# Performance work log

Measured on AMD Instinct MI355X. Metric: run time of the kernel, lower is better.

## Reference

```python
import jax, jax.numpy as jnp
import numpy as np

SEQ, INP, BOND, BATCH = 256, 4, 128, 2048


def setup_inputs() -> dict:
    key = jax.random.key(0)
    k1, k2, k3 = jax.random.split(key, 3)
    # near-eye init: identity plus small noise (matches near_eye_init intent)
    eye = jnp.eye(BOND, dtype=jnp.float32)
    core_tensors = eye[None, None] + 0.01 * jax.random.normal(k1, (SEQ, INP, BOND, BOND), dtype=jnp.float32)
    edge_vecs = jax.random.normal(k2, (2, BOND), dtype=jnp.float32) / np.float32(np.sqrt(BOND))
    input_data = jax.random.randint(k3, (SEQ, BATCH), 0, INP)
    return {"input_data": input_data, "core_tensors": core_tensors, "edge_vecs": edge_vecs}


def reference(input_data, core_tensors, edge_vecs):
    """log P(x) = 2*log|h_n^T omega| - log Z for an open-boundary real MPS.

    h_t = A_t[x_t] h_{t-1}, h_0 = alpha.
    Z tracked via density-matrix recurrence M_t = sum_i A_t[i] M_{t-1} A_t[i]^T,
    M_0 = alpha alpha^T, Z = omega^T M_n omega.
    Log-scaling on both scans prevents under/overflow.
    """
    alpha, omega = edge_vecs[0], edge_vecs[1]
    B = input_data.shape[1]
    D = core_tensors.shape[2]

    # ---- amplitude scan over sequence (batched D-dim matvecs) ----
    def amp_step(carry, inp):
        h, logn = carry            # h: [B, D], logn: [B]
        A_t, x_t = inp             # A_t: [I, D, D], x_t: [B]
        mats = A_t[x_t]            # [B, D, D] gather of per-token core slices
        h = jnp.einsum('bij,bj->bi', mats, h)
        s = jnp.linalg.norm(h, axis=-1, keepdims=True)
        return (h / s, logn + jnp.log(s[:, 0])), None

    h0 = jnp.broadcast_to(alpha, (B, D))
    (h, logn), _ = jax.lax.scan(amp_step, (h0, jnp.zeros((B,), h0.dtype)),
                                (core_tensors, input_data))
    amp = h @ omega                                   # [B]
    log_amp_sq = 2.0 * (jnp.log(jnp.abs(amp)) + logn)

    # ---- normalization scan (transfer-matrix / density-matrix form) ----
    def z_step(carry, A_t):
        M, logz = carry            # M: [D, D]
        M = jnp.einsum('iab,bc,idc->ad', A_t, M, A_t)  # sum_i A_i M A_i^T
        s = jnp.linalg.norm(M)
        return (M / s, logz + jnp.log(s)), None

    M0 = jnp.outer(alpha, alpha)
    (M, logz), _ = jax.lax.scan(z_step, (M0, jnp.zeros((), M0.dtype)), core_tensors)
    log_Z = jnp.log(omega @ M @ omega) + logz

    return log_amp_sq - log_Z
```

## Files before the change

### kernel.cpp

```cpp
#include <hip/hip_runtime.h>
#include <cstdint>
#include <cstddef>

#define SEQ   256
#define INP   4
#define BOND  128
#define BATCH 2048
#define MATSZ (BOND*BOND)

typedef __bf16 bf16x8 __attribute__((ext_vector_type(8)));
typedef __bf16 bf16x4 __attribute__((ext_vector_type(4)));
typedef float  f32x4  __attribute__((ext_vector_type(4)));
typedef short  s16x4  __attribute__((ext_vector_type(4)));

static constexpr size_t SZ_MAT   = (size_t)SEQ*INP*MATSZ*2;
static constexpr size_t OFF_ABF  = 0;
static constexpr size_t OFF_ATBF = OFF_ABF + SZ_MAT;
static constexpr size_t OFF_BHI  = OFF_ATBF + SZ_MAT;
static constexpr size_t OFF_BLO  = OFF_BHI + SZ_MAT;
static constexpr size_t SZ_MWS   = 2ull*MATSZ*2;
static constexpr size_t SZ_TAIL  = SZ_MWS + (size_t)BATCH*4 + 64;

static __device__ __forceinline__ unsigned short f2bf(float f) {
    union { float f; uint32_t u; } v; v.f = f;
    uint32_t r = (v.u + 0x7FFFu + ((v.u >> 16) & 1u)) >> 16;
    return (unsigned short)r;
}
static __device__ __forceinline__ float bf2f(unsigned short b) {
    union { uint32_t u; float f; } v; v.u = ((uint32_t)b) << 16;
    return v.f;
}
static __device__ __forceinline__ f32x4 mfma16(bf16x8 a, bf16x8 b, f32x4 c) {
    return __builtin_amdgcn_mfma_f32_16x16x32_bf16(a, b, c, 0, 0, 0);
}
#if defined(__has_builtin)
#if __has_builtin(__builtin_amdgcn_mfma_f32_16x16x16bf16_1k)
#define HAVE_MFMA16X16_BUILTIN 1
#endif
#endif
static __device__ __forceinline__ f32x4 mfma16x16(bf16x4 a, bf16x4 b, f32x4 c) {
#ifdef HAVE_MFMA16X16_BUILTIN
    return __builtin_amdgcn_mfma_f32_16x16x16bf16_1k(
        __builtin_bit_cast(s16x4, a), __builtin_bit_cast(s16x4, b), c, 0, 0, 0);
#else
    asm("v_mfma_f32_16x16x16_bf16 %0, %1, %2, %0" : "+v"(c) : "v"(a), "v"(b));
    return c;
#endif
}
static __device__ __forceinline__ unsigned int cvtpk(float a, float b) {
    unsigned int d;
    asm("v_cvt_pk_bf16_f32 %0, %1, %2" : "=v"(d) : "v"(a), "v"(b));
    return d;
}
static __device__ __forceinline__ int xoff(int r, int c8) {
    return ((r << 4) + (c8 ^ (r & 15))) << 3;
}
static __device__ __forceinline__ void gload_lds16(const unsigned short* g, unsigned short* l) {
    __builtin_amdgcn_global_load_lds((const __attribute__((address_space(1))) unsigned int*)g,
                                     (__attribute__((address_space(3))) unsigned int*)l,
                                     16, 0, 0);
}
static __device__ __forceinline__ void stage_mat(const unsigned short* __restrict__ Ai,
                                                 unsigned short* dst, int tid) {
#pragma unroll
    for (int j = 0; j < 4; ++j) {
        int slot = j * 512 + tid;
        int r = slot >> 4, c8 = slot & 15;
        const unsigned short* src = Ai + (size_t)r * BOND + ((c8 ^ (r & 15)) << 3);
        unsigned short* ldst = dst + (size_t)(j * 512 + (tid & ~63)) * 8;
        gload_lds16(src, ldst);
    }
}

__global__ void convert_kernel(const float* __restrict__ core,
                               unsigned short* __restrict__ abf,
                               unsigned short* __restrict__ atbf,
                               unsigned short* __restrict__ bhi,
                               unsigned short* __restrict__ blo,
                               int use_blo) {
    __shared__ unsigned short tile[BOND][BOND + 2];
    const int mat = blockIdx.x;
    const float* src = core + (size_t)mat * MATSZ;
    unsigned short* dA = abf  + (size_t)mat * MATSZ;
    unsigned short* dT = atbf + (size_t)mat * MATSZ;
    unsigned short* dH = bhi  + (size_t)mat * MATSZ;
    unsigned short* dL = blo  + (size_t)mat * MATSZ;
    const int tid = threadIdx.x;
    for (int j = 0; j < 16; ++j) {
        int lin4 = (tid + j * 256) * 4;
        float4 f = *(const float4*)(src + lin4);
        int r = lin4 >> 7, c = lin4 & 127;
        unsigned short a0=f2bf(f.x), a1=f2bf(f.y), a2=f2bf(f.z), a3=f2bf(f.w);
        *(ushort4*)(dA + lin4) = make_ushort4(a0,a1,a2,a3);
        tile[r][c]=a0; tile[r][c+1]=a1; tile[r][c+2]=a2; tile[r][c+3]=a3;
        float b0 = f.x - ((r == c    ) ? 1.0f : 0.0f);
        float b1 = f.y - ((r == c + 1) ? 1.0f : 0.0f);
        float b2 = f.z - ((r == c + 2) ? 1.0f : 0.0f);
        float b3 = f.w - ((r == c + 3) ? 1.0f : 0.0f);
        unsigned short h0=f2bf(b0), h1=f2bf(b1), h2=f2bf(b2), h3=f2bf(b3);
        *(ushort4*)(dH + lin4) = make_ushort4(h0,h1,h2,h3);
        if (use_blo) {
            *(ushort4*)(dL + lin4) = make_ushort4(
                f2bf(b0 - bf2f(h0)), f2bf(b1 - bf2f(h1)),
                f2bf(b2 - bf2f(h2)), f2bf(b3 - bf2f(h3)));
        }
    }
    __syncthreads();
    for (int j = 0; j < 16; ++j) {
        int lin4 = (tid + j * 256) * 4;
        int co = lin4 >> 7, r0 = lin4 & 127;
        *(ushort4*)(dT + lin4) = make_ushort4(tile[r0][co], tile[r0+1][co],
                                              tile[r0+2][co], tile[r0+3][co]);
    }
}

struct ZSm {
    unsigned short As[2][MATSZ];
    unsigned short M[MATSZ];
    float vec[BOND];
};
struct ASm2 {
    int   toks[SEQ * 32];
    unsigned short hhi[32 * BOND];
    unsigned short hlo[32 * BOND];
    float partial[8][32];
    float sinv[32];
    float logn[32];
};
union SmU { ZSm z; ASm2 a; };

template<int USE_BLO>
__global__ __launch_bounds__(512)
__attribute__((amdgpu_waves_per_eu(2, 2)))
void main_kernel(
        const int*   __restrict__ xdata,
        const float* __restrict__ edge,
        const unsigned short* __restrict__ abf,
        const unsigned short* __restrict__ atbf,
        const unsigned short* __restrict__ bhi,
        const unsigned short* __restrict__ blo,
        unsigned short* __restrict__ mws,
        float* __restrict__ logamp) {
    __shared__ SmU sm;
    const int tid = threadIdx.x;
    const int l   = tid & 63;
    const int w   = tid >> 6;
    const int lo  = l & 15;
    const int hi  = l >> 4;

    if (blockIdx.x < 2) {
        const int chain = blockIdx.x;
        const unsigned short* Abase = chain ? atbf : abf;

        if (tid < BOND) sm.z.vec[tid] = edge[chain * BOND + tid];
        __syncthreads();
        for (int idx = tid; idx < MATSZ; idx += 512) {
            int r = idx >> 7, c = idx & 127;
            sm.z.M[xoff(r, c >> 3) + (c & 7)] = f2bf(sm.z.vec[r] * sm.z.vec[c]);
        }
        stage_mat(Abase + (size_t)(chain ? (SEQ - 1) : 0) * INP * MATSZ, sm.z.As[0], tid);
        __syncthreads();

        int cur = 0;
        for (int s = 1; s <= 128; ++s) {
            const int tstep = chain ? (SEQ - s) : (s - 1);
            const unsigned short* As_g = Abase + (size_t)tstep * INP * MATSZ;
            f32x4 accM[2][8];
#pragma unroll
            for (int mt = 0; mt < 2; ++mt)
#pragma unroll
                for (int ct = 0; ct < 8; ++ct) accM[mt][ct] = (f32x4){0.f, 0.f, 0.f, 0.f};

            for (int i = 0; i < 4; ++i) {
                const unsigned short* nxt = nullptr;
                if (i < 3)           nxt = As_g + (size_t)(i + 1) * MATSZ;
                else if (s < 128)    nxt = Abase + (size_t)(chain ? (SEQ - s - 1) : s) * INP * MATSZ;
                if (nxt) stage_mat(nxt, sm.z.As[cur ^ 1], tid);

                if (w < 4) {
                    __builtin_amdgcn_s_setprio(1);
                    const unsigned short* Ac = sm.z.As[cur];
                    f32x4 acc1[8][2];
#pragma unroll
                    for (int pt = 0; pt < 8; ++pt) {
                        acc1[pt][0] = (f32x4){0.f, 0.f, 0.f, 0.f};
                        acc1[pt][1] = (f32x4){0.f, 0.f, 0.f, 0.f};
                    }
#pragma unroll
                    for (int kk = 0; kk < 4; ++kk) {
                        bf16x8 bq0 = *(const bf16x8*)&Ac[xoff(w * 32 + lo,      kk * 4 + hi)];
                        bf16x8 bq1 = *(const bf16x8*)&Ac[xoff(w * 32 + 16 + lo, kk * 4 + hi)];
#pragma unroll
                        for (int pt = 0; pt < 8; ++pt) {
                            bf16x8 mf = *(const bf16x8*)&sm.z.M[xoff(pt * 16 + lo, kk * 4 + hi)];
                            acc1[pt][0] = mfma16(mf, bq0, acc1[pt][0]);
                            acc1[pt][1] = mfma16(mf, bq1, acc1[pt][1]);
                        }
                    }
                    bf16x4 tf[2][8];
#pragma unroll
                    for (int pt = 0; pt < 8; ++pt)
#pragma unroll
                        for (int mt = 0; mt < 2; ++mt) {
                            union { unsigned int u[2]; bf16x4 v; } pk;
                            pk.u[0] = cvtpk(acc1[pt][mt][0], acc1[pt][mt][1]);
                            pk.u[1] = cvtpk(acc1[pt][mt][2], acc1[pt][mt][3]);
                            tf[mt][pt] = pk.v;
                        }
#pragma unroll
                    for (int ks = 0; ks < 8; ++ks) {
#pragma unroll
                        for (int ct = 0; ct < 8; ++ct) {
                            bf16x4 bb = *(const bf16x4*)&Ac[xoff(ct * 16 + lo, 2 * ks + (hi >> 1)) + 4 * (hi & 1)];
                            accM[0][ct] = mfma16x16(tf[0][ks], bb, accM[0][ct]);
                            accM[1][ct] = mfma16x16(tf[1][ks], bb, accM[1][ct]);
                        }
                    }
                    __builtin_amdgcn_s_setprio(0);
                }
                asm volatile("s_waitcnt vmcnt(0)" ::: "memory");
                __builtin_amdgcn_s_barrier();
                cur ^= 1;
            }
            if (w < 4) {
#pragma unroll
                for (int mt = 0; mt < 2; ++mt)
#pragma unroll
                    for (int ct = 0; ct < 8; ++ct)
#pragma unroll
                        for (int r = 0; r < 4; ++r) {
                            int row = w * 32 + mt * 16 + hi * 4 + r;
                            int col = ct * 16 + lo;
                            sm.z.M[xoff(row, col >> 3) + (col & 7)] =
                                f2bf(accM[mt][ct][r] * 0.25f);
                        }
            }
            asm volatile("s_waitcnt lgkmcnt(0)" ::: "memory");
            __builtin_amdgcn_s_barrier();
        }
        unsigned short* outb = mws + (size_t)chain * MATSZ;
        for (int j = 0; j < 4; ++j) {
            int chunk = tid + j * 512;
            int r = chunk >> 4, c8 = chunk & 15;
            *(bf16x8*)(outb + (size_t)r * BOND + c8 * 8) =
                *(const bf16x8*)&sm.z.M[xoff(r, c8)];
        }
    } else {
        const int lr = lo, lq = hi;
        const int b0 = (blockIdx.x - 2) * 32;

        for (int j = 0; j < 16; ++j) {
            int idx = tid + j * 512;
            int t = idx >> 5, c = idx & 31;
            sm.a.toks[idx] = xdata[(size_t)t * BATCH + b0 + c];
        }
        if (tid < 32) sm.a.logn[tid] = 0.f;
        for (int idx = tid; idx < 32 * BOND; idx += 512) {
            int c = idx >> 7, r = idx & 127;
            float v = edge[r];
            unsigned short hb = f2bf(v);
            int si = xoff(c, r >> 3) + (r & 7);
            sm.a.hhi[si] = hb;
            sm.a.hlo[si] = f2bf(v - bf2f(hb));
        }
        f32x4 al = *(const f32x4*)(edge + w * 16 + lq * 4);
        f32x4 hreg0 = al, hreg1 = al;
        __syncthreads();

        const size_t ro = (size_t)(w * 16 + lr) * BOND + lq * 8;

        bf16x8 bvh[4][4], bvl[4][4];
#pragma unroll
        for (int v = 0; v < 4; ++v)
#pragma unroll
            for (int kk = 0; kk < 4; ++kk) {
                bvh[v][kk] = *(const bf16x8*)(bhi + (size_t)v * MATSZ + ro + kk * 32);
                if (USE_BLO) bvl[v][kk] = *(const bf16x8*)(blo + (size_t)v * MATSZ + ro + kk * 32);
            }

        for (int t = 0; t < SEQ; ++t) {
            bf16x8 hh0[4], hh1[4], hl0[4], hl1[4];
#pragma unroll
            for (int kk = 0; kk < 4; ++kk) {
                hh0[kk] = *(const bf16x8*)&sm.a.hhi[xoff(lr,      kk * 4 + lq)];
                hh1[kk] = *(const bf16x8*)&sm.a.hhi[xoff(16 + lr, kk * 4 + lq)];
                hl0[kk] = *(const bf16x8*)&sm.a.hlo[xoff(lr,      kk * 4 + lq)];
                hl1[kk] = *(const bf16x8*)&sm.a.hlo[xoff(16 + lr, kk * 4 + lq)];
            }
            f32x4 acc[4][2];
#pragma unroll
            for (int v = 0; v < 4; ++v) {
                acc[v][0] = (f32x4){0.f, 0.f, 0.f, 0.f};
                acc[v][1] = (f32x4){0.f, 0.f, 0.f, 0.f};
            }
            const unsigned short* BhN = bhi + (size_t)(t + 1) * INP * MATSZ + ro;
            const unsigned short* BlN = blo + (size_t)(t + 1) * INP * MATSZ + ro;
#pragma unroll
            for (int v = 0; v < 4; ++v) {
#pragma unroll
                for (int kk = 0; kk < 4; ++kk) {
                    acc[v][0] = mfma16(bvh[v][kk], hh0[kk], acc[v][0]);
                    acc[v][0] = mfma16(bvh[v][kk], hl0[kk], acc[v][0]);
                    acc[v][1] = mfma16(bvh[v][kk], hh1[kk], acc[v][1]);
                    acc[v][1] = mfma16(bvh[v][kk], hl1[kk], acc[v][1]);
                    if (USE_BLO) {
                        acc[v][0] = mfma16(bvl[v][kk], hh0[kk], acc[v][0]);
                        acc[v][1] = mfma16(bvl[v][kk], hh1[kk], acc[v][1]);
                    }
                }
                if (t < SEQ - 1) {
#pragma unroll
                    for (int kk = 0; kk < 4; ++kk) {
                        bvh[v][kk] = *(const bf16x8*)(BhN + (size_t)v * MATSZ + kk * 32);
                        if (USE_BLO) bvl[v][kk] = *(const bf16x8*)(BlN + (size_t)v * MATSZ + kk * 32);
                    }
                }
            }
            int tokA = sm.a.toks[t * 32 + lr];
            int tokB = sm.a.toks[t * 32 + 16 + lr];
            f32x4 d0 = acc[0][0];
            d0 = (tokA == 1) ? acc[1][0] : d0;
            d0 = (tokA == 2) ? acc[2][0] : d0;
            d0 = (tokA == 3) ? acc[3][0] : d0;
            f32x4 d1 = acc[0][1];
            d1 = (tokB == 1) ? acc[1][1] : d1;
            d1 = (tokB == 2) ? acc[2][1] : d1;
            d1 = (tokB == 3) ? acc[3][1] : d1;
            f32x4 h2_0 = hreg0 + d0;
            f32x4 h2_1 = hreg1 + d1;

            if ((t & 7) == 7) {
                float ss0 = h2_0[0]*h2_0[0] + h2_0[1]*h2_0[1] + h2_0[2]*h2_0[2] + h2_0[3]*h2_0[3];
                ss0 += __shfl_xor(ss0, 16);
                ss0 += __shfl_xor(ss0, 32);
                float ss1 = h2_1[0]*h2_1[0] + h2_1[1]*h2_1[1] + h2_1[2]*h2_1[2] + h2_1[3]*h2_1[3];
                ss1 += __shfl_xor(ss1, 16);
                ss1 += __shfl_xor(ss1, 32);
                if (lq == 0) {
                    sm.a.partial[w][lr]      = ss0;
                    sm.a.partial[w][16 + lr] = ss1;
                }
                __syncthreads();
                if (tid < 32) {
                    float s2 = 0.f;
#pragma unroll
                    for (int w2 = 0; w2 < 8; ++w2) s2 += sm.a.partial[w2][tid];
                    sm.a.sinv[tid] = rsqrtf(s2);
                    sm.a.logn[tid] += 0.5f * logf(s2);
                }
                __syncthreads();
                h2_0 *= sm.a.sinv[lr];
                h2_1 *= sm.a.sinv[16 + lr];
            }
            hreg0 = h2_0;
            hreg1 = h2_1;
            __syncthreads();
#pragma unroll
            for (int ct = 0; ct < 2; ++ct) {
                f32x4 hv = (ct == 0) ? h2_0 : h2_1;
                int c = ct * 16 + lr;
                unsigned short q0 = f2bf(hv[0]), q1 = f2bf(hv[1]),
                               q2 = f2bf(hv[2]), q3 = f2bf(hv[3]);
                int c8w = w * 2 + (lq >> 1);
                int si  = xoff(c, c8w) + (lq & 1) * 4;
                *(ushort4*)&sm.a.hhi[si] = make_ushort4(q0, q1, q2, q3);
                *(ushort4*)&sm.a.hlo[si] =
                    make_ushort4(f2bf(hv[0] - bf2f(q0)), f2bf(hv[1] - bf2f(q1)),
                                 f2bf(hv[2] - bf2f(q2)), f2bf(hv[3] - bf2f(q3)));
            }
            __syncthreads();
        }
        f32x4 og = *(const f32x4*)(edge + BOND + w * 16 + lq * 4);
#pragma unroll
        for (int ct = 0; ct < 2; ++ct) {
            f32x4 hv = (ct == 0) ? hreg0 : hreg1;
            float ss = hv[0]*og[0] + hv[1]*og[1] + hv[2]*og[2] + hv[3]*og[3];
            ss += __shfl_xor(ss, 16);
            ss += __shfl_xor(ss, 32);
            if (lq == 0) sm.a.partial[w][ct * 16 + lr] = ss;
        }
        __syncthreads();
        if (tid < 32) {
            float dot = 0.f;
#pragma unroll
            for (int w2 = 0; w2 < 8; ++w2) dot += sm.a.partial[w2][tid];
            logamp[b0 + tid] = 2.f * (logf(fabsf(dot)) + sm.a.logn[tid]);
        }
    }
}

__global__ __launch_bounds__(1024) void fin_kernel(const unsigned short* __restrict__ mws,
                                                   const float* __restrict__ logamp,
                                                   float* __restrict__ out) {
    __shared__ float red[1024];
    const int tid = threadIdx.x;
    const unsigned short* Sf = mws;
    const unsigned short* Rb = mws + MATSZ;
    float part = 0.f;
    for (int j = 0; j < 16; ++j) {
        int idx = tid + j * 1024;
        part += bf2f(Sf[idx]) * bf2f(Rb[idx]);
    }
    red[tid] = part;
    __syncthreads();
    for (int off = 512; off > 0; off >>= 1) {
        if (tid < off) red[tid] += red[tid + off];
        __syncthreads();
    }
    float lz = logf(red[0]) + 256.0f * 1.3862943611198906f;
    out[tid]        = logamp[tid]        - lz;
    out[tid + 1024] = logamp[tid + 1024] - lz;
}

extern "C" void kernel_launch(void* const* d_in, const int* in_sizes, int n_in,
                              void* d_out, int out_size, void* d_ws, size_t ws_size,
                              hipStream_t stream) {
    const int*   xdata = (const int*)d_in[0];
    const float* core  = (const float*)d_in[1];
    const float* edge  = (const float*)d_in[2];
    float* out = (float*)d_out;
    char* ws = (char*)d_ws;

    const size_t need_full  = OFF_BLO + SZ_MAT + SZ_TAIL;
    const size_t need_noblo = OFF_BLO + SZ_TAIL;
    const int use_blo = (ws_size >= need_full) ? 1 : 0;
    if (!use_blo && ws_size < need_noblo) return;

    unsigned short* abf  = (unsigned short*)(ws + OFF_ABF);
    unsigned short* atbf = (unsigned short*)(ws + OFF_ATBF);
    unsigned short* bhi  = (unsigned short*)(ws + OFF_BHI);
    unsigned short* blo  = (unsigned short*)(ws + (use_blo ? OFF_BLO : OFF_BHI));
    const size_t tail = use_blo ? (OFF_BLO + SZ_MAT) : OFF_BLO;
    unsigned short* mws  = (unsigned short*)(ws + tail);
    float* logamp = (float*)(ws + tail + SZ_MWS);

    convert_kernel<<<SEQ * INP, 256, 0, stream>>>(core, abf, atbf, bhi, blo, use_blo);
    if (use_blo)
        main_kernel<1><<<66, 512, 0, stream>>>(xdata, edge, abf, atbf, bhi, blo, mws, logamp);
    else
        main_kernel<0><<<66, 512, 0, stream>>>(xdata, edge, abf, atbf, bhi, blo, mws, logamp);
    fin_kernel<<<1, 1024, 0, stream>>>(mws, logamp, out);
}
```

Before: 2.447 ms.

## Triple-buffer Z-chain core staging with software-pipelined GEMMs and halve amplitude batch tile

The density-matrix chain now keeps three shared-memory staging buffers, prefetches two matrices ahead, and software-pipelines the next matrix's first GEMM (M·A) behind the current matrix's second GEMM. The goal is to shorten the serial critical path of the two Z blocks, which bound total runtime. Separately, the amplitude blocks now handle 16 batch columns instead of 32, so the launch grows from 66 to 130 blocks and spreads across more CUs. The trade-offs are more shared memory per Z block and more global reads of the B matrices per batch element, since each block re-reads them for fewer columns.

```diff
diff --git a/kernel.cpp b/kernel.cpp
--- a/kernel.cpp
+++ b/kernel.cpp
@@ -115,17 +115,17 @@
 }
 
 struct ZSm {
-    unsigned short As[2][MATSZ];
+    unsigned short As[3][MATSZ];
     unsigned short M[MATSZ];
     float vec[BOND];
 };
 struct ASm2 {
-    int   toks[SEQ * 32];
-    unsigned short hhi[32 * BOND];
-    unsigned short hlo[32 * BOND];
-    float partial[8][32];
-    float sinv[32];
-    float logn[32];
+    int   toks[SEQ * 16];
+    unsigned short hhi[16 * BOND];
+    unsigned short hlo[16 * BOND];
+    float partial[8][16];
+    float sinv[16];
+    float logn[16];
 };
 union SmU { ZSm z; ASm2 a; };
 
@@ -152,75 +152,85 @@
         const int chain = blockIdx.x;
         const unsigned short* Abase = chain ? atbf : abf;
 
+        auto tokptr = [&](int g) -> const unsigned short* {
+            int ts = chain ? (SEQ - 1 - (g >> 2)) : (g >> 2);
+            return Abase + ((size_t)ts * INP + (g & 3)) * MATSZ;
+        };
+
         if (tid < BOND) sm.z.vec[tid] = edge[chain * BOND + tid];
         __syncthreads();
         for (int idx = tid; idx < MATSZ; idx += 512) {
             int r = idx >> 7, c = idx & 127;
             sm.z.M[xoff(r, c >> 3) + (c & 7)] = f2bf(sm.z.vec[r] * sm.z.vec[c]);
         }
-        stage_mat(Abase + (size_t)(chain ? (SEQ - 1) : 0) * INP * MATSZ, sm.z.As[0], tid);
+        unsigned short *pb0 = sm.z.As[0], *pb1 = sm.z.As[1], *pb2 = sm.z.As[2];
+        stage_mat(tokptr(0), pb0, tid);
+        stage_mat(tokptr(1), pb1, tid);
         __syncthreads();
 
-        int cur = 0;
+        f32x4 accM[2][8];
+        bf16x4 tf[2][8];
+
+        auto P1 = [&](const unsigned short* Ac) {
+            f32x4 acc1[8][2];
+#pragma unroll
+            for (int pt = 0; pt < 8; ++pt) {
+                acc1[pt][0] = (f32x4){0.f, 0.f, 0.f, 0.f};
+                acc1[pt][1] = (f32x4){0.f, 0.f, 0.f, 0.f};
+            }
+#pragma unroll
+            for (int kk = 0; kk < 4; ++kk) {
+                bf16x8 bq0 = *(const bf16x8*)&Ac[xoff(w * 32 + lo,      kk * 4 + hi)];
+                bf16x8 bq1 = *(const bf16x8*)&Ac[xoff(w * 32 + 16 + lo, kk * 4 + hi)];
+#pragma unroll
+                for (int pt = 0; pt < 8; ++pt) {
+                    bf16x8 mf = *(const bf16x8*)&sm.z.M[xoff(pt * 16 + lo, kk * 4 + hi)];
+                    acc1[pt][0] = mfma16(mf, bq0, acc1[pt][0]);
+                    acc1[pt][1] = mfma16(mf, bq1, acc1[pt][1]);
+                }
+            }
+#pragma unroll
+            for (int pt = 0; pt < 8; ++pt)
+#pragma unroll
+                for (int mt = 0; mt < 2; ++mt) {
+                    union { unsigned int u[2]; bf16x4 v; } pk;
+                    pk.u[0] = cvtpk(acc1[pt][mt][0], acc1[pt][mt][1]);
+                    pk.u[1] = cvtpk(acc1[pt][mt][2], acc1[pt][mt][3]);
+                    tf[mt][pt] = pk.v;
+                }
+        };
+        auto P2 = [&](const unsigned short* Ac) {
+#pragma unroll
+            for (int ks = 0; ks < 8; ++ks) {
+#pragma unroll
+                for (int ct = 0; ct < 8; ++ct) {
+                    bf16x4 bb = *(const bf16x4*)&Ac[xoff(ct * 16 + lo, 2 * ks + (hi >> 1)) + 4 * (hi & 1)];
+                    accM[0][ct] = mfma16x16(tf[0][ks], bb, accM[0][ct]);
+                    accM[1][ct] = mfma16x16(tf[1][ks], bb, accM[1][ct]);
+                }
+            }
+        };
+
+        if (w < 4) P1(pb0);
+
         for (int s = 1; s <= 128; ++s) {
-            const int tstep = chain ? (SEQ - s) : (s - 1);
-            const unsigned short* As_g = Abase + (size_t)tstep * INP * MATSZ;
-            f32x4 accM[2][8];
 #pragma unroll
             for (int mt = 0; mt < 2; ++mt)
 #pragma unroll
                 for (int ct = 0; ct < 8; ++ct) accM[mt][ct] = (f32x4){0.f, 0.f, 0.f, 0.f};
 
             for (int i = 0; i < 4; ++i) {
-                const unsigned short* nxt = nullptr;
-                if (i < 3)           nxt = As_g + (size_t)(i + 1) * MATSZ;
-                else if (s < 128)    nxt = Abase + (size_t)(chain ? (SEQ - s - 1) : s) * INP * MATSZ;
-                if (nxt) stage_mat(nxt, sm.z.As[cur ^ 1], tid);
-
+                const int g = (s - 1) * 4 + i;
+                if (g + 2 < 512) stage_mat(tokptr(g + 2), pb2, tid);
                 if (w < 4) {
                     __builtin_amdgcn_s_setprio(1);
-                    const unsigned short* Ac = sm.z.As[cur];
-                    f32x4 acc1[8][2];
-#pragma unroll
-                    for (int pt = 0; pt < 8; ++pt) {
-                        acc1[pt][0] = (f32x4){0.f, 0.f, 0.f, 0.f};
-                        acc1[pt][1] = (f32x4){0.f, 0.f, 0.f, 0.f};
-                    }
-#pragma unroll
-                    for (int kk = 0; kk < 4; ++kk) {
-                        bf16x8 bq0 = *(const bf16x8*)&Ac[xoff(w * 32 + lo,      kk * 4 + hi)];
-                        bf16x8 bq1 = *(const bf16x8*)&Ac[xoff(w * 32 + 16 + lo, kk * 4 + hi)];
-#pragma unroll
-                        for (int pt = 0; pt < 8; ++pt) {
-                            bf16x8 mf = *(const bf16x8*)&sm.z.M[xoff(pt * 16 + lo, kk * 4 + hi)];
-                            acc1[pt][0] = mfma16(mf, bq0, acc1[pt][0]);
-                            acc1[pt][1] = mfma16(mf, bq1, acc1[pt][1]);
-                        }
-                    }
-                    bf16x4 tf[2][8];
-#pragma unroll
-                    for (int pt = 0; pt < 8; ++pt)
-#pragma unroll
-                        for (int mt = 0; mt < 2; ++mt) {
-                            union { unsigned int u[2]; bf16x4 v; } pk;
-                            pk.u[0] = cvtpk(acc1[pt][mt][0], acc1[pt][mt][1]);
-                            pk.u[1] = cvtpk(acc1[pt][mt][2], acc1[pt][mt][3]);
-                            tf[mt][pt] = pk.v;
-                        }
-#pragma unroll
-                    for (int ks = 0; ks < 8; ++ks) {
-#pragma unroll
-                        for (int ct = 0; ct < 8; ++ct) {
-                            bf16x4 bb = *(const bf16x4*)&Ac[xoff(ct * 16 + lo, 2 * ks + (hi >> 1)) + 4 * (hi & 1)];
-                            accM[0][ct] = mfma16x16(tf[0][ks], bb, accM[0][ct]);
-                            accM[1][ct] = mfma16x16(tf[1][ks], bb, accM[1][ct]);
-                        }
-                    }
+                    P2(pb0);
+                    if (i < 3) P1(pb1);
                     __builtin_amdgcn_s_setprio(0);
                 }
                 asm volatile("s_waitcnt vmcnt(0)" ::: "memory");
                 __builtin_amdgcn_s_barrier();
-                cur ^= 1;
+                unsigned short* tpp = pb0; pb0 = pb1; pb1 = pb2; pb2 = tpp;
             }
             if (w < 4) {
 #pragma unroll
@@ -237,6 +247,7 @@
             }
             asm volatile("s_waitcnt lgkmcnt(0)" ::: "memory");
             __builtin_amdgcn_s_barrier();
+            if (s < 128 && w < 4) P1(pb0);
         }
         unsigned short* outb = mws + (size_t)chain * MATSZ;
         for (int j = 0; j < 4; ++j) {
@@ -247,15 +258,15 @@
         }
     } else {
         const int lr = lo, lq = hi;
-        const int b0 = (blockIdx.x - 2) * 32;
-
-        for (int j = 0; j < 16; ++j) {
+        const int b0 = (blockIdx.x - 2) * 16;
+
+        for (int j = 0; j < 8; ++j) {
             int idx = tid + j * 512;
-            int t = idx >> 5, c = idx & 31;
+            int t = idx >> 4, c = idx & 15;
             sm.a.toks[idx] = xdata[(size_t)t * BATCH + b0 + c];
         }
-        if (tid < 32) sm.a.logn[tid] = 0.f;
-        for (int idx = tid; idx < 32 * BOND; idx += 512) {
+        if (tid < 16) sm.a.logn[tid] = 0.f;
+        for (int idx = tid; idx < 16 * BOND; idx += 512) {
             int c = idx >> 7, r = idx & 127;
             float v = edge[r];
             unsigned short hb = f2bf(v);
@@ -264,7 +275,7 @@
             sm.a.hlo[si] = f2bf(v - bf2f(hb));
         }
         f32x4 al = *(const f32x4*)(edge + w * 16 + lq * 4);
-        f32x4 hreg0 = al, hreg1 = al;
+        f32x4 hreg0 = al;
         __syncthreads();
 
         const size_t ro = (size_t)(w * 16 + lr) * BOND + lq * 8;
@@ -279,34 +290,24 @@
             }
 
         for (int t = 0; t < SEQ; ++t) {
-            bf16x8 hh0[4], hh1[4], hl0[4], hl1[4];
+            bf16x8 hh0[4], hl0[4];
 #pragma unroll
             for (int kk = 0; kk < 4; ++kk) {
-                hh0[kk] = *(const bf16x8*)&sm.a.hhi[xoff(lr,      kk * 4 + lq)];
-                hh1[kk] = *(const bf16x8*)&sm.a.hhi[xoff(16 + lr, kk * 4 + lq)];
-                hl0[kk] = *(const bf16x8*)&sm.a.hlo[xoff(lr,      kk * 4 + lq)];
-                hl1[kk] = *(const bf16x8*)&sm.a.hlo[xoff(16 + lr, kk * 4 + lq)];
-            }
-            f32x4 acc[4][2];
-#pragma unroll
-            for (int v = 0; v < 4; ++v) {
-                acc[v][0] = (f32x4){0.f, 0.f, 0.f, 0.f};
-                acc[v][1] = (f32x4){0.f, 0.f, 0.f, 0.f};
-            }
+                hh0[kk] = *(const bf16x8*)&sm.a.hhi[xoff(lr, kk * 4 + lq)];
+                hl0[kk] = *(const bf16x8*)&sm.a.hlo[xoff(lr, kk * 4 + lq)];
+            }
+            f32x4 acc[4];
+#pragma unroll
+            for (int v = 0; v < 4; ++v) acc[v] = (f32x4){0.f, 0.f, 0.f, 0.f};
             const unsigned short* BhN = bhi + (size_t)(t + 1) * INP * MATSZ + ro;
             const unsigned short* BlN = blo + (size_t)(t + 1) * INP * MATSZ + ro;
 #pragma unroll
             for (int v = 0; v < 4; ++v) {
 #pragma unroll
                 for (int kk = 0; kk < 4; ++kk) {
-                    acc[v][0] = mfma16(bvh[v][kk], hh0[kk], acc[v][0]);
-                    acc[v][0] = mfma16(bvh[v][kk], hl0[kk], acc[v][0]);
-                    acc[v][1] = mfma16(bvh[v][kk], hh1[kk], acc[v][1]);
-                    acc[v][1] = mfma16(bvh[v][kk], hl1[kk], acc[v][1]);
-                    if (USE_BLO) {
-                        acc[v][0] = mfma16(bvl[v][kk], hh0[kk], acc[v][0]);
-                        acc[v][1] = mfma16(bvl[v][kk], hh1[kk], acc[v][1]);
-                    }
+                    acc[v] = mfma16(bvh[v][kk], hh0[kk], acc[v]);
+                    acc[v] = mfma16(bvh[v][kk], hl0[kk], acc[v]);
+                    if (USE_BLO) acc[v] = mfma16(bvl[v][kk], hh0[kk], acc[v]);
                 }
                 if (t < SEQ - 1) {
 #pragma unroll
@@ -316,32 +317,20 @@
                     }
                 }
             }
-            int tokA = sm.a.toks[t * 32 + lr];
-            int tokB = sm.a.toks[t * 32 + 16 + lr];
-            f32x4 d0 = acc[0][0];
-            d0 = (tokA == 1) ? acc[1][0] : d0;
-            d0 = (tokA == 2) ? acc[2][0] : d0;
-            d0 = (tokA == 3) ? acc[3][0] : d0;
-            f32x4 d1 = acc[0][1];
-            d1 = (tokB == 1) ? acc[1][1] : d1;
-            d1 = (tokB == 2) ? acc[2][1] : d1;
-            d1 = (tokB == 3) ? acc[3][1] : d1;
+            int tokA = sm.a.toks[t * 16 + lr];
+            f32x4 d0 = acc[0];
+            d0 = (tokA == 1) ? acc[1] : d0;
+            d0 = (tokA == 2) ? acc[2] : d0;
+            d0 = (tokA == 3) ? acc[3] : d0;
             f32x4 h2_0 = hreg0 + d0;
-            f32x4 h2_1 = hreg1 + d1;
 
             if ((t & 7) == 7) {
                 float ss0 = h2_0[0]*h2_0[0] + h2_0[1]*h2_0[1] + h2_0[2]*h2_0[2] + h2_0[3]*h2_0[3];
                 ss0 += __shfl_xor(ss0, 16);
                 ss0 += __shfl_xor(ss0, 32);
-                float ss1 = h2_1[0]*h2_1[0] + h2_1[1]*h2_1[1] + h2_1[2]*h2_1[2] + h2_1[3]*h2_1[3];
-                ss1 += __shfl_xor(ss1, 16);
-                ss1 += __shfl_xor(ss1, 32);
-                if (lq == 0) {
-                    sm.a.partial[w][lr]      = ss0;
-                    sm.a.partial[w][16 + lr] = ss1;
-                }
+                if (lq == 0) sm.a.partial[w][lr] = ss0;
                 __syncthreads();
-                if (tid < 32) {
+                if (tid < 16) {
                     float s2 = 0.f;
 #pragma unroll
                     for (int w2 = 0; w2 < 8; ++w2) s2 += sm.a.partial[w2][tid];
@@ -350,37 +339,31 @@
                 }
                 __syncthreads();
                 h2_0 *= sm.a.sinv[lr];
-                h2_1 *= sm.a.sinv[16 + lr];
             }
             hreg0 = h2_0;
-            hreg1 = h2_1;
             __syncthreads();
-#pragma unroll
-            for (int ct = 0; ct < 2; ++ct) {
-                f32x4 hv = (ct == 0) ? h2_0 : h2_1;
-                int c = ct * 16 + lr;
-                unsigned short q0 = f2bf(hv[0]), q1 = f2bf(hv[1]),
-                               q2 = f2bf(hv[2]), q3 = f2bf(hv[3]);
+            {
+                int c = lr;
+                unsigned short q0 = f2bf(h2_0[0]), q1 = f2bf(h2_0[1]),
+                               q2 = f2bf(h2_0[2]), q3 = f2bf(h2_0[3]);
                 int c8w = w * 2 + (lq >> 1);
                 int si  = xoff(c, c8w) + (lq & 1) * 4;
                 *(ushort4*)&sm.a.hhi[si] = make_ushort4(q0, q1, q2, q3);
                 *(ushort4*)&sm.a.hlo[si] =
-                    make_ushort4(f2bf(hv[0] - bf2f(q0)), f2bf(hv[1] - bf2f(q1)),
-                                 f2bf(hv[2] - bf2f(q2)), f2bf(hv[3] - bf2f(q3)));
+                    make_ushort4(f2bf(h2_0[0] - bf2f(q0)), f2bf(h2_0[1] - bf2f(q1)),
+                                 f2bf(h2_0[2] - bf2f(q2)), f2bf(h2_0[3] - bf2f(q3)));
             }
             __syncthreads();
         }
         f32x4 og = *(const f32x4*)(edge + BOND + w * 16 + lq * 4);
-#pragma unroll
-        for (int ct = 0; ct < 2; ++ct) {
-            f32x4 hv = (ct == 0) ? hreg0 : hreg1;
-            float ss = hv[0]*og[0] + hv[1]*og[1] + hv[2]*og[2] + hv[3]*og[3];
+        {
+            float ss = hreg0[0]*og[0] + hreg0[1]*og[1] + hreg0[2]*og[2] + hreg0[3]*og[3];
             ss += __shfl_xor(ss, 16);
             ss += __shfl_xor(ss, 32);
-            if (lq == 0) sm.a.partial[w][ct * 16 + lr] = ss;
+            if (lq == 0) sm.a.partial[w][lr] = ss;
         }
         __syncthreads();
-        if (tid < 32) {
+        if (tid < 16) {
             float dot = 0.f;
 #pragma unroll
             for (int w2 = 0; w2 < 8; ++w2) dot += sm.a.partial[w2][tid];
@@ -436,8 +419,8 @@
 
     convert_kernel<<<SEQ * INP, 256, 0, stream>>>(core, abf, atbf, bhi, blo, use_blo);
     if (use_blo)
-        main_kernel<1><<<66, 512, 0, stream>>>(xdata, edge, abf, atbf, bhi, blo, mws, logamp);
+        main_kernel<1><<<130, 512, 0, stream>>>(xdata, edge, abf, atbf, bhi, blo, mws, logamp);
     else
-        main_kernel<0><<<66, 512, 0, stream>>>(xdata, edge, abf, atbf, bhi, blo, mws, logamp);
+        main_kernel<0><<<130, 512, 0, stream>>>(xdata, edge, abf, atbf, bhi, blo, mws, logamp);
     fin_kernel<<<1, 1024, 0, stream>>>(mws, logamp, out);
 }
```

Result: faster. 2.049 ms, median of 2 (-16.3%).
